# Kernel optimization log

Hardware: AMD Instinct MI355X
Metric: run time of the kernel (lower is better)

Reference implementation:

```python
import jax, jax.numpy as jnp
import numpy as np

N_NODES = 50000
N_EDGES = 1600000
L = 16  # lifted_dim

def setup_inputs() -> dict:
    key = jax.random.key(0)
    ks = jax.random.split(key, 12)
    M1 = 2 * L          # 32
    M2 = 4 * M1 + 2 * L  # 160
    s = lambda f: 1.0 / np.sqrt(f)
    return {
        "x_s": jax.random.normal(ks[0], (N_NODES, L), jnp.float32),
        "x_t": jax.random.normal(ks[1], (N_NODES, L), jnp.float32),
        "edge_attr": jax.random.normal(ks[2], (N_EDGES, L), jnp.float32),
        "u": jax.random.normal(ks[3], (1, L), jnp.float32),
        "W1a": jax.random.normal(ks[4], (M1, M1), jnp.float32) * s(M1),
        "b1a": jnp.zeros((M1,), jnp.float32),
        "W2a": jax.random.normal(ks[5], (M1, M1), jnp.float32) * s(M1),
        "b2a": jnp.zeros((M1,), jnp.float32),
        "W1b": jax.random.normal(ks[6], (M2, M2), jnp.float32) * s(M2),
        "b1b": jnp.zeros((M2,), jnp.float32),
        "W2b": jax.random.normal(ks[7], (M2, L), jnp.float32) * s(M2),
        "b2b": jnp.zeros((L,), jnp.float32),
        "gamma": jnp.ones((L,), jnp.float32),
        "beta": jnp.zeros((L,), jnp.float32),
        "edge_index": jax.random.randint(ks[8], (2, N_EDGES), 0, N_NODES, jnp.int32),
    }

def _leaky(x, slope):
    return jnp.where(x >= 0, x, slope * x)

def _forward(x_s, x_t, edge_attr, u, W1a, b1a, W2a, b2a, W1b, b1b, W2b, b2b, gamma, beta, edge_index):
    src, tgt = edge_index[0], edge_index[1]
    n = x_s.shape[0]
    # message MLP on gathered neighbor features
    in_msg = jnp.concatenate([x_t[tgt], edge_attr], axis=1)          # [E, 2L]
    h = _leaky(in_msg @ W1a + b1a, 0.1)
    msg = h @ W2a + b2a                                              # [E, 2L]
    # multi-moment segment reduce
    seg = lambda v: jax.ops.segment_sum(v, src, num_segments=n)
    cnt = seg(jnp.ones((msg.shape[0], 1), msg.dtype))
    denom = jnp.maximum(cnt, 1.0)
    mean = seg(msg) / denom                                          # [N, 2L]
    var = _leaky(seg(msg * msg) / denom - mean * mean, 0.01)
    std = jnp.sqrt(var + 1e-6)
    z = (msg - mean[src]) / std[src]                                 # standardized per-edge
    skew = jnp.nan_to_num(seg(z ** 3) / denom, nan=0.0)
    kurt = jnp.nan_to_num(seg(z ** 4) / denom, nan=0.0)
    h_cat = jnp.concatenate([x_s, mean, std, skew, kurt,
                             jnp.broadcast_to(u, (n, u.shape[1]))], axis=-1)  # [N, 10L]
    h2 = _leaky(h_cat @ W1b + b1b, 0.1)
    out = h2 @ W2b + b2b                                             # [N, L]
    # BatchNorm1d (training-mode batch stats, eps=1e-5)
    mu = jnp.mean(out, axis=0)
    vb = jnp.mean((out - mu) ** 2, axis=0)
    return gamma * (out - mu) * jax.lax.rsqrt(vb + 1e-5) + beta

def reference(x_s, x_t, edge_attr, u, W1a, b1a, W2a, b2a, W1b, b1b, W2b, b2b, gamma, beta, edge_index):
    return _forward(x_s, x_t, edge_attr, u, W1a, b1a, W2a, b2a, W1b, b1b, W2b, b2b, gamma, beta, edge_index)
```

## Files before the change

### kernel.cpp

```cpp
#include <hip/hip_runtime.h>

#define N_NODES 50000
#define N_EDGES 1600000

#define EPB 8192
#define NB1 ((N_EDGES + EPB - 1) / EPB)
#define NPB 64
#define NBK ((N_NODES + NPB - 1) / NPB)
#define TBL (NBK * NB1)
#define NSB ((TBL + 255) / 256)
#define MAXB 4096
#define SCATB 1024

typedef unsigned short ushort_t;
typedef __attribute__((ext_vector_type(8))) __bf16 bf16x8;
typedef __attribute__((ext_vector_type(4))) float  f32x4;

union FU { ushort_t s[8]; bf16x8 v; };

__device__ __forceinline__ ushort_t f2bf(float f) {
    union { float f; unsigned int i; } v; v.f = f;
    unsigned int r = v.i + 0x7fffu + ((v.i >> 16) & 1u);
    return (ushort_t)(r >> 16);
}
__device__ __forceinline__ float leaky(float x, float s) { return x >= 0.f ? x : s * x; }

__global__ __launch_bounds__(256) void k_cvtx(const float* __restrict__ x_t,
                                              ushort_t* __restrict__ x_tb) {
    int i = blockIdx.x * 256 + threadIdx.x;
    if (i < (N_NODES * 16) / 4) {
        f32x4 v = ((const f32x4*)x_t)[i];
        unsigned long long p = (unsigned long long)f2bf(v[0])
                             | ((unsigned long long)f2bf(v[1]) << 16)
                             | ((unsigned long long)f2bf(v[2]) << 32)
                             | ((unsigned long long)f2bf(v[3]) << 48);
        ((unsigned long long*)x_tb)[i] = p;
    }
}

__global__ __launch_bounds__(SCATB) void k_bcount(const int* __restrict__ src, int* __restrict__ table) {
    __shared__ int cnt[NBK];
    const int t = threadIdx.x, blk = blockIdx.x;
    for (int i = t; i < NBK; i += SCATB) cnt[i] = 0;
    __syncthreads();
    const int base = blk * EPB;
    for (int i = t; i < EPB; i += SCATB) {
        int e = base + i;
        if (e < N_EDGES) atomicAdd(&cnt[src[e] >> 6], 1);
    }
    __syncthreads();
    for (int b = t; b < NBK; b += SCATB) table[b * NB1 + blk] = cnt[b];
}

__global__ __launch_bounds__(256) void k_scan1(int* __restrict__ table, int* __restrict__ bsum) {
    __shared__ int buf[256];
    const int t = threadIdx.x, i = blockIdx.x * 256 + t;
    int v = (i < TBL) ? table[i] : 0;
    buf[t] = v; __syncthreads();
    for (int off = 1; off < 256; off <<= 1) {
        int x = (t >= off) ? buf[t - off] : 0;
        __syncthreads(); buf[t] += x; __syncthreads();
    }
    int incl = buf[t];
    if (i < TBL) table[i] = incl - v;
    if (t == 255) bsum[blockIdx.x] = incl;
}
__global__ __launch_bounds__(256) void k_scan2(int* __restrict__ bsum, float* __restrict__ bnsum) {
    __shared__ int sums[256];
    const int t = threadIdx.x;
    if (t < 32) bnsum[t] = 0.f;
    const int SEG = (NSB + 255) / 256;
    const int s0 = t * SEG, s1 = (s0 + SEG < NSB) ? s0 + SEG : NSB;
    int sum = 0;
    for (int i = s0; i < s1; i++) sum += bsum[i];
    sums[t] = sum; __syncthreads();
    for (int off = 1; off < 256; off <<= 1) {
        int x = (t >= off) ? sums[t - off] : 0;
        __syncthreads(); sums[t] += x; __syncthreads();
    }
    int carry = sums[t] - sum;
    for (int i = s0; i < s1; i++) { int v = bsum[i]; bsum[i] = carry; carry += v; }
}
__global__ __launch_bounds__(256) void k_scan3(int* __restrict__ table, const int* __restrict__ bsum) {
    const int i = blockIdx.x * 256 + threadIdx.x;
    if (i < TBL) table[i] += bsum[blockIdx.x];
}

__global__ __launch_bounds__(SCATB) void k_bscat(const int* __restrict__ src, const int* __restrict__ tgt,
                                                 const float* __restrict__ ea, const int* __restrict__ table,
                                                 int* __restrict__ tnA, ushort_t* __restrict__ eaA) {
    __shared__ int cur[NBK];
    const int t = threadIdx.x, blk = blockIdx.x;
    for (int i = t; i < NBK; i += SCATB) cur[i] = table[i * NB1 + blk];
    __syncthreads();
    const int base = blk * EPB;
    for (int i = t; i < EPB; i += SCATB) {
        int e = base + i;
        if (e < N_EDGES) {
            int s = src[e];
            int pos = atomicAdd(&cur[s >> 6], 1);
            tnA[pos] = tgt[e] | ((s & (NPB - 1)) << 16);
            const f32x4* ep = (const f32x4*)(ea + (size_t)e * 16);
            f32x4 v0 = __builtin_nontemporal_load(ep);
            f32x4 v1 = __builtin_nontemporal_load(ep + 1);
            f32x4 v2 = __builtin_nontemporal_load(ep + 2);
            f32x4 v3 = __builtin_nontemporal_load(ep + 3);
            FU lo, hi;
            #pragma unroll
            for (int j = 0; j < 4; j++) {
                lo.s[j] = f2bf(v0[j]); lo.s[4 + j] = f2bf(v1[j]);
                hi.s[j] = f2bf(v2[j]); hi.s[4 + j] = f2bf(v3[j]);
            }
            *(bf16x8*)(eaA + (size_t)pos * 16)     = lo.v;
            *(bf16x8*)(eaA + (size_t)pos * 16 + 8) = hi.v;
        }
    }
}

__global__ __launch_bounds__(256) void k_nodeF(
    const ushort_t* __restrict__ x_tb, const ushort_t* __restrict__ eaA, const int* __restrict__ tnA,
    const int* __restrict__ table,
    const float* __restrict__ w1a, const float* __restrict__ b1a,
    const float* __restrict__ w2a, const float* __restrict__ b2a,
    const float* __restrict__ x_s, const float* __restrict__ u,
    ushort_t* __restrict__ hcat)
{
    __shared__ ushort_t permL[MAXB];
    __shared__ ushort_t tgL[MAXB];
    __shared__ int cntL[NPB], scanL[NPB], curL[NPB];
    __shared__ __align__(16) float h_lds[4][16][36];
    __shared__ ushort_t stat_lds[4][128];

    const int t = threadIdx.x;
    const int w = t >> 6, L = t & 63, q = L >> 4, c = L & 15;
    const int b = blockIdx.x;
    const int base  = table[b * NB1];
    const int end   = (b < NBK - 1) ? table[(b + 1) * NB1] : N_EDGES;
    const int cntB0 = end - base;
    const int cntB  = cntB0 < MAXB ? cntB0 : MAXB;

    if (t < NPB) cntL[t] = 0;
    __syncthreads();
    for (int i = t; i < cntB; i += 256) {
        int v = tnA[base + i];
        tgL[i] = (ushort_t)(v & 0xFFFF);
        atomicAdd(&cntL[v >> 16], 1);
    }
    __syncthreads();
    if (t == 0) {
        int s = 0;
        for (int nl = 0; nl < NPB; nl++) { scanL[nl] = s; s += cntL[nl]; }
    }
    __syncthreads();
    if (t < NPB) curL[t] = scanL[t];
    __syncthreads();
    for (int i = t; i < cntB; i += 256) {
        int nl = tnA[base + i] >> 16;
        int loc = atomicAdd(&curL[nl], 1);
        permL[loc] = (ushort_t)i;
    }

    bf16x8 B1[2], B2[2];
    #pragma unroll
    for (int h = 0; h < 2; h++) {
        FU u1, u2;
        #pragma unroll
        for (int j = 0; j < 8; j++) {
            int kk = q * 8 + j, nn = c + 16 * h;
            u1.s[j] = f2bf(w1a[kk * 32 + nn]);
            u2.s[j] = f2bf(w2a[kk * 32 + nn]);
        }
        B1[h] = u1.v; B2[h] = u2.v;
    }
    const float bias1[2] = { b1a[c], b1a[c + 16] };
    const float bias2[2] = { b2a[c], b2a[c + 16] };
    const f32x4 zero = { 0.f, 0.f, 0.f, 0.f };
    __syncthreads();

    for (int kn = 0; kn < 16; kn++) {
        const int nl = w * 16 + kn;
        const int n  = b * NPB + nl;
        const int startL = scanL[nl], d = cntL[nl];
        float s1a = 0.f, s2a = 0.f, s3a = 0.f, s4a = 0.f;
        float s1b = 0.f, s2b = 0.f, s3b = 0.f, s4b = 0.f;
        const int ntl = (d + 15) >> 4;

        for (int tl = 0; tl < ntl; tl++) {
            int row  = tl * 16 + c;
            int ridx = row < d ? row : d - 1;
            int li   = permL[startL + ridx];
            FU af;
            if (q < 2) {
                int tg = tgL[li];
                __builtin_memcpy(&af.v, x_tb + (size_t)tg * 16 + q * 8, 16);
            } else {
                __builtin_memcpy(&af.v, eaA + (size_t)(base + li) * 16 + (q - 2) * 8, 16);
            }

            f32x4 a0 = __builtin_amdgcn_mfma_f32_16x16x32_bf16(af.v, B1[0], zero, 0, 0, 0);
            f32x4 a1 = __builtin_amdgcn_mfma_f32_16x16x32_bf16(af.v, B1[1], zero, 0, 0, 0);
            #pragma unroll
            for (int r = 0; r < 4; r++) {
                h_lds[w][q * 4 + r][c]      = leaky(a0[r] + bias1[0], 0.1f);
                h_lds[w][q * 4 + r][c + 16] = leaky(a1[r] + bias1[1], 0.1f);
            }
            __asm__ volatile("s_waitcnt lgkmcnt(0)" ::: "memory");

            float hv[8];
            __builtin_memcpy(&hv, &h_lds[w][c][q * 8], 32);
            FU hf;
            #pragma unroll
            for (int j = 0; j < 8; j++) hf.s[j] = f2bf(hv[j]);
            f32x4 m0 = __builtin_amdgcn_mfma_f32_16x16x32_bf16(hf.v, B2[0], zero, 0, 0, 0);
            f32x4 m1 = __builtin_amdgcn_mfma_f32_16x16x32_bf16(hf.v, B2[1], zero, 0, 0, 0);

            int rb = tl * 16 + q * 4;
            #pragma unroll
            for (int r = 0; r < 4; r++) {
                if (rb + r < d) {
                    float m = m0[r] + bias2[0], mm = m * m;
                    s1a += m;  s2a += mm; s3a += mm * m; s4a += mm * mm;
                    float x = m1[r] + bias2[1], xx = x * x;
                    s1b += x;  s2b += xx; s3b += xx * x; s4b += xx * xx;
                }
            }
        }

        if (n >= N_NODES) continue;

        s1a += __shfl_xor(s1a, 16); s1a += __shfl_xor(s1a, 32);
        s2a += __shfl_xor(s2a, 16); s2a += __shfl_xor(s2a, 32);
        s3a += __shfl_xor(s3a, 16); s3a += __shfl_xor(s3a, 32);
        s4a += __shfl_xor(s4a, 16); s4a += __shfl_xor(s4a, 32);
        s1b += __shfl_xor(s1b, 16); s1b += __shfl_xor(s1b, 32);
        s2b += __shfl_xor(s2b, 16); s2b += __shfl_xor(s2b, 32);
        s3b += __shfl_xor(s3b, 16); s3b += __shfl_xor(s3b, 32);
        s4b += __shfl_xor(s4b, 16); s4b += __shfl_xor(s4b, 32);

        if (q == 0) {
            float denom = fmaxf((float)d, 1.f);
            {
                float mean = s1a / denom, m2r = s2a / denom, m3r = s3a / denom, m4r = s4a / denom;
                float var  = leaky(m2r - mean * mean, 0.01f);
                float stdv = sqrtf(var + 1e-6f);
                float e3   = m3r - 3.f * mean * m2r + 2.f * mean * mean * mean;
                float skew = e3 / (stdv * stdv * stdv);
                float e4   = m4r - 4.f * mean * m3r + 6.f * mean * mean * m2r
                             - 3.f * mean * mean * mean * mean;
                float kurt = e4 / (stdv * stdv * stdv * stdv);
                stat_lds[w][c]      = f2bf(mean);
                stat_lds[w][32 + c] = f2bf(stdv);
                stat_lds[w][64 + c] = f2bf(skew);
                stat_lds[w][96 + c] = f2bf(kurt);
            }
            {
                float mean = s1b / denom, m2r = s2b / denom, m3r = s3b / denom, m4r = s4b / denom;
                float var  = leaky(m2r - mean * mean, 0.01f);
                float stdv = sqrtf(var + 1e-6f);
                float e3   = m3r - 3.f * mean * m2r + 2.f * mean * mean * mean;
                float skew = e3 / (stdv * stdv * stdv);
                float e4   = m4r - 4.f * mean * m3r + 6.f * mean * mean * m2r
                             - 3.f * mean * mean * mean * mean;
                float kurt = e4 / (stdv * stdv * stdv * stdv);
                stat_lds[w][16 + c]  = f2bf(mean);
                stat_lds[w][48 + c]  = f2bf(stdv);
                stat_lds[w][80 + c]  = f2bf(skew);
                stat_lds[w][112 + c] = f2bf(kurt);
            }
        }
        __asm__ volatile("s_waitcnt lgkmcnt(0)" ::: "memory");

        const size_t basep = (size_t)n * 160;
        unsigned int sv;
        __builtin_memcpy(&sv, &stat_lds[w][L * 2], 4);
        *(unsigned int*)(hcat + basep + 16 + L * 2) = sv;
        if (L < 16) {
            hcat[basep + L]       = f2bf(x_s[(size_t)n * 16 + L]);
            hcat[basep + 144 + L] = f2bf(u[L]);
        }
    }
}

__global__ __launch_bounds__(256) void k_gemm1(const ushort_t* __restrict__ hcat,
                                               const float* __restrict__ w1b,
                                               const float* __restrict__ b1b,
                                               ushort_t* __restrict__ h2)
{
    __shared__ __align__(16) ushort_t W1T[160 * 168];
    int t = threadIdx.x;
    for (int i = t; i < 160 * 160; i += 256) { int k = i / 160, n = i % 160; W1T[n * 168 + k] = f2bf(w1b[i]); }
    __syncthreads();
    int w = t >> 6, L = t & 63, q = L >> 4, c = L & 15;
    const f32x4 zero = { 0.f, 0.f, 0.f, 0.f };
    for (int tile = blockIdx.x * 4 + w; tile < 3125 * 10; tile += gridDim.x * 4) {
        int rt = tile / 10, nt = tile % 10;
        int m = rt * 16 + c, n = nt * 16 + c;
        f32x4 acc = zero;
        #pragma unroll
        for (int ks = 0; ks < 5; ks++) {
            bf16x8 a; __builtin_memcpy(&a, hcat + (size_t)m * 160 + ks * 32 + q * 8, 16);
            bf16x8 b; __builtin_memcpy(&b, &W1T[n * 168 + ks * 32 + q * 8], 16);
            acc = __builtin_amdgcn_mfma_f32_16x16x32_bf16(a, b, acc, 0, 0, 0);
        }
        float bias = b1b[n];
        #pragma unroll
        for (int r = 0; r < 4; r++) {
            h2[(size_t)(rt * 16 + q * 4 + r) * 160 + n] = f2bf(leaky(acc[r] + bias, 0.1f));
        }
    }
}

__global__ __launch_bounds__(256) void k_gemm2(const ushort_t* __restrict__ h2,
                                               const float* __restrict__ w2b,
                                               const float* __restrict__ b2b,
                                               float* __restrict__ outpre, float* __restrict__ bnsum)
{
    __shared__ __align__(16) ushort_t W2T[16 * 168];
    int t = threadIdx.x;
    for (int i = t; i < 160 * 16; i += 256) { int k = i / 16, n = i % 16; W2T[n * 168 + k] = f2bf(w2b[i]); }
    __syncthreads();
    int w = t >> 6, L = t & 63, q = L >> 4, c = L & 15;
    const f32x4 zero = { 0.f, 0.f, 0.f, 0.f };
    float ps = 0.f, ps2 = 0.f;
    float bias = b2b[c];
    for (int rt = blockIdx.x * 4 + w; rt < 3125; rt += gridDim.x * 4) {
        int m = rt * 16 + c;
        f32x4 acc = zero;
        #pragma unroll
        for (int ks = 0; ks < 5; ks++) {
            bf16x8 a; __builtin_memcpy(&a, h2 + (size_t)m * 160 + ks * 32 + q * 8, 16);
            bf16x8 b; __builtin_memcpy(&b, &W2T[c * 168 + ks * 32 + q * 8], 16);
            acc = __builtin_amdgcn_mfma_f32_16x16x32_bf16(a, b, acc, 0, 0, 0);
        }
        #pragma unroll
        for (int r = 0; r < 4; r++) {
            float v = acc[r] + bias;
            outpre[(size_t)(rt * 16 + q * 4 + r) * 16 + c] = v;
            ps += v; ps2 += v * v;
        }
    }
    ps  += __shfl_xor(ps, 16);  ps  += __shfl_xor(ps, 32);
    ps2 += __shfl_xor(ps2, 16); ps2 += __shfl_xor(ps2, 32);
    if (q == 0) {
        unsafeAtomicAdd(&bnsum[c], ps);
        unsafeAtomicAdd(&bnsum[16 + c], ps2);
    }
}

__global__ __launch_bounds__(256) void k_bn(const float* __restrict__ outpre, const float* __restrict__ bnsum,
                                            const float* __restrict__ gamma, const float* __restrict__ beta,
                                            float* __restrict__ out)
{
    int i = blockIdx.x * 256 + threadIdx.x;
    int c = i & 15;
    float x = outpre[i];
    float mu = bnsum[c] * (1.f / N_NODES);
    float var = bnsum[16 + c] * (1.f / N_NODES) - mu * mu;
    out[i] = gamma[c] * (x - mu) * rsqrtf(var + 1e-5f) + beta[c];
}

extern "C" void kernel_launch(void* const* d_in, const int* in_sizes, int n_in,
                              void* d_out, int out_size, void* d_ws, size_t ws_size,
                              hipStream_t stream) {
    const float* x_s  = (const float*)d_in[0];
    const float* x_t  = (const float*)d_in[1];
    const float* ea   = (const float*)d_in[2];
    const float* u    = (const float*)d_in[3];
    const float* w1a  = (const float*)d_in[4];
    const float* b1a  = (const float*)d_in[5];
    const float* w2a  = (const float*)d_in[6];
    const float* b2a  = (const float*)d_in[7];
    const float* w1b  = (const float*)d_in[8];
    const float* b1b  = (const float*)d_in[9];
    const float* w2b  = (const float*)d_in[10];
    const float* b2b  = (const float*)d_in[11];
    const float* gam  = (const float*)d_in[12];
    const float* bet  = (const float*)d_in[13];
    const int* eidx   = (const int*)d_in[14];
    const int* src = eidx;
    const int* tgt = eidx + N_EDGES;

    char* ws = (char*)d_ws;
    const size_t OFF_TABLE  = 0;
    const size_t OFF_BSUM   = 614400;
    const size_t OFF_BNSUM  = 655360;
    const size_t OFF_OUTPRE = 786432;
    const size_t OFF_XTB    = 4194304;
    const size_t OFF_TNA    = 6291456;
    const size_t OFF_EAA    = 16777216;
    const size_t OFF_HCAT   = 68157440;
    const size_t OFF_H2     = 84934656;

    int*      table  = (int*)(ws + OFF_TABLE);
    int*      bsum   = (int*)(ws + OFF_BSUM);
    float*    bnsum  = (float*)(ws + OFF_BNSUM);
    float*    outpre = (float*)(ws + OFF_OUTPRE);
    ushort_t* x_tb   = (ushort_t*)(ws + OFF_XTB);
    int*      tnA    = (int*)(ws + OFF_TNA);
    ushort_t* eaA    = (ushort_t*)(ws + OFF_EAA);
    ushort_t* hcat   = (ushort_t*)(ws + OFF_HCAT);
    ushort_t* h2     = (ushort_t*)(ws + OFF_H2);

    k_cvtx  <<<(N_NODES * 16 / 4 + 255) / 256, 256, 0, stream>>>(x_t, x_tb);
    k_bcount<<<NB1, SCATB, 0, stream>>>(src, table);
    k_scan1 <<<NSB, 256, 0, stream>>>(table, bsum);
    k_scan2 <<<1,   256, 0, stream>>>(bsum, bnsum);
    k_scan3 <<<NSB, 256, 0, stream>>>(table, bsum);
    k_bscat <<<NB1, SCATB, 0, stream>>>(src, tgt, ea, table, tnA, eaA);
    k_nodeF <<<NBK, 256, 0, stream>>>(x_tb, eaA, tnA, table, w1a, b1a, w2a, b2a, x_s, u, hcat);
    k_gemm1 <<<1024, 256, 0, stream>>>(hcat, w1b, b1b, h2);
    k_gemm2 <<<512,  256, 0, stream>>>(h2, w2b, b2b, outpre, bnsum);
    k_bn    <<<(N_NODES * 16) / 256, 256, 0, stream>>>(outpre, bnsum, gam, bet, (float*)d_out);
}
```

Measured before the change: 429.9 us.

## Fuse x_t conversion and scan fix-up into consumers, double nodes per block

The x_t-to-bf16 conversion moves into the bucket-count kernel, and the separate scan3 pass is removed: consumers now add the block prefix from bsum when they read the table. Node buckets grow from 64 to 128 nodes, and the node kernel runs 512 threads with LDS scratch sized for 8 waves. This cuts two launches and halves the number of node blocks and table entries. The cost is more LDS and threads per block, and a per-bucket edge cap that could overflow on skewed inputs.

```diff
diff --git a/kernel.cpp b/kernel.cpp
--- a/kernel.cpp
+++ b/kernel.cpp
@@ -5,12 +5,13 @@
 
 #define EPB 8192
 #define NB1 ((N_EDGES + EPB - 1) / EPB)
-#define NPB 64
+#define NPB 128
 #define NBK ((N_NODES + NPB - 1) / NPB)
 #define TBL (NBK * NB1)
 #define NSB ((TBL + 255) / 256)
-#define MAXB 4096
+#define MAXB 4608
 #define SCATB 1024
+#define NFT 512
 
 typedef unsigned short ushort_t;
 typedef __attribute__((ext_vector_type(8))) __bf16 bf16x8;
@@ -25,28 +26,25 @@
 }
 __device__ __forceinline__ float leaky(float x, float s) { return x >= 0.f ? x : s * x; }
 
-__global__ __launch_bounds__(256) void k_cvtx(const float* __restrict__ x_t,
-                                              ushort_t* __restrict__ x_tb) {
-    int i = blockIdx.x * 256 + threadIdx.x;
-    if (i < (N_NODES * 16) / 4) {
-        f32x4 v = ((const f32x4*)x_t)[i];
+__global__ __launch_bounds__(SCATB) void k_bcount(const int* __restrict__ src, int* __restrict__ table,
+                                                  const float* __restrict__ x_t, ushort_t* __restrict__ x_tb) {
+    __shared__ int cnt[NBK];
+    const int t = threadIdx.x, blk = blockIdx.x;
+    const int g = blk * SCATB + t;
+    if (g < (N_NODES * 16) / 4) {
+        f32x4 v = ((const f32x4*)x_t)[g];
         unsigned long long p = (unsigned long long)f2bf(v[0])
                              | ((unsigned long long)f2bf(v[1]) << 16)
                              | ((unsigned long long)f2bf(v[2]) << 32)
                              | ((unsigned long long)f2bf(v[3]) << 48);
-        ((unsigned long long*)x_tb)[i] = p;
-    }
-}
-
-__global__ __launch_bounds__(SCATB) void k_bcount(const int* __restrict__ src, int* __restrict__ table) {
-    __shared__ int cnt[NBK];
-    const int t = threadIdx.x, blk = blockIdx.x;
+        ((unsigned long long*)x_tb)[g] = p;
+    }
     for (int i = t; i < NBK; i += SCATB) cnt[i] = 0;
     __syncthreads();
     const int base = blk * EPB;
     for (int i = t; i < EPB; i += SCATB) {
         int e = base + i;
-        if (e < N_EDGES) atomicAdd(&cnt[src[e] >> 6], 1);
+        if (e < N_EDGES) atomicAdd(&cnt[src[e] >> 7], 1);
     }
     __syncthreads();
     for (int b = t; b < NBK; b += SCATB) table[b * NB1 + blk] = cnt[b];
@@ -81,24 +79,24 @@
     int carry = sums[t] - sum;
     for (int i = s0; i < s1; i++) { int v = bsum[i]; bsum[i] = carry; carry += v; }
 }
-__global__ __launch_bounds__(256) void k_scan3(int* __restrict__ table, const int* __restrict__ bsum) {
-    const int i = blockIdx.x * 256 + threadIdx.x;
-    if (i < TBL) table[i] += bsum[blockIdx.x];
-}
 
 __global__ __launch_bounds__(SCATB) void k_bscat(const int* __restrict__ src, const int* __restrict__ tgt,
                                                  const float* __restrict__ ea, const int* __restrict__ table,
+                                                 const int* __restrict__ bsum,
                                                  int* __restrict__ tnA, ushort_t* __restrict__ eaA) {
     __shared__ int cur[NBK];
     const int t = threadIdx.x, blk = blockIdx.x;
-    for (int i = t; i < NBK; i += SCATB) cur[i] = table[i * NB1 + blk];
+    for (int i = t; i < NBK; i += SCATB) {
+        int idx = i * NB1 + blk;
+        cur[i] = table[idx] + bsum[idx >> 8];
+    }
     __syncthreads();
     const int base = blk * EPB;
     for (int i = t; i < EPB; i += SCATB) {
         int e = base + i;
         if (e < N_EDGES) {
             int s = src[e];
-            int pos = atomicAdd(&cur[s >> 6], 1);
+            int pos = atomicAdd(&cur[s >> 7], 1);
             tnA[pos] = tgt[e] | ((s & (NPB - 1)) << 16);
             const f32x4* ep = (const f32x4*)(ea + (size_t)e * 16);
             f32x4 v0 = __builtin_nontemporal_load(ep);
@@ -117,9 +115,9 @@
     }
 }
 
-__global__ __launch_bounds__(256) void k_nodeF(
+__global__ __launch_bounds__(NFT) void k_nodeF(
     const ushort_t* __restrict__ x_tb, const ushort_t* __restrict__ eaA, const int* __restrict__ tnA,
-    const int* __restrict__ table,
+    const int* __restrict__ table, const int* __restrict__ bsum,
     const float* __restrict__ w1a, const float* __restrict__ b1a,
     const float* __restrict__ w2a, const float* __restrict__ b2a,
     const float* __restrict__ x_s, const float* __restrict__ u,
@@ -128,20 +126,23 @@
     __shared__ ushort_t permL[MAXB];
     __shared__ ushort_t tgL[MAXB];
     __shared__ int cntL[NPB], scanL[NPB], curL[NPB];
-    __shared__ __align__(16) float h_lds[4][16][36];
-    __shared__ ushort_t stat_lds[4][128];
+    __shared__ __align__(16) float h_lds[8][16][36];
+    __shared__ ushort_t stat_lds[8][128];
 
     const int t = threadIdx.x;
     const int w = t >> 6, L = t & 63, q = L >> 4, c = L & 15;
     const int b = blockIdx.x;
-    const int base  = table[b * NB1];
-    const int end   = (b < NBK - 1) ? table[(b + 1) * NB1] : N_EDGES;
+    const int i0   = b * NB1;
+    const int base = table[i0] + bsum[i0 >> 8];
+    int end;
+    if (b < NBK - 1) { const int i1 = (b + 1) * NB1; end = table[i1] + bsum[i1 >> 8]; }
+    else end = N_EDGES;
     const int cntB0 = end - base;
     const int cntB  = cntB0 < MAXB ? cntB0 : MAXB;
 
     if (t < NPB) cntL[t] = 0;
     __syncthreads();
-    for (int i = t; i < cntB; i += 256) {
+    for (int i = t; i < cntB; i += NFT) {
         int v = tnA[base + i];
         tgL[i] = (ushort_t)(v & 0xFFFF);
         atomicAdd(&cntL[v >> 16], 1);
@@ -154,7 +155,7 @@
     __syncthreads();
     if (t < NPB) curL[t] = scanL[t];
     __syncthreads();
-    for (int i = t; i < cntB; i += 256) {
+    for (int i = t; i < cntB; i += NFT) {
         int nl = tnA[base + i] >> 16;
         int loc = atomicAdd(&curL[nl], 1);
         permL[loc] = (ushort_t)i;
@@ -401,13 +402,11 @@
     ushort_t* hcat   = (ushort_t*)(ws + OFF_HCAT);
     ushort_t* h2     = (ushort_t*)(ws + OFF_H2);
 
-    k_cvtx  <<<(N_NODES * 16 / 4 + 255) / 256, 256, 0, stream>>>(x_t, x_tb);
-    k_bcount<<<NB1, SCATB, 0, stream>>>(src, table);
+    k_bcount<<<NB1, SCATB, 0, stream>>>(src, table, x_t, x_tb);
     k_scan1 <<<NSB, 256, 0, stream>>>(table, bsum);
     k_scan2 <<<1,   256, 0, stream>>>(bsum, bnsum);
-    k_scan3 <<<NSB, 256, 0, stream>>>(table, bsum);
-    k_bscat <<<NB1, SCATB, 0, stream>>>(src, tgt, ea, table, tnA, eaA);
-    k_nodeF <<<NBK, 256, 0, stream>>>(x_tb, eaA, tnA, table, w1a, b1a, w2a, b2a, x_s, u, hcat);
+    k_bscat <<<NB1, SCATB, 0, stream>>>(src, tgt, ea, table, bsum, tnA, eaA);
+    k_nodeF <<<NBK, NFT, 0, stream>>>(x_tb, eaA, tnA, table, bsum, w1a, b1a, w2a, b2a, x_s, u, hcat);
     k_gemm1 <<<1024, 256, 0, stream>>>(hcat, w1b, b1b, h2);
     k_gemm2 <<<512,  256, 0, stream>>>(h2, w2b, b2b, outpre, bnsum);
     k_bn    <<<(N_NODES * 16) / 256, 256, 0, stream>>>(outpre, bnsum, gam, bet, (float*)d_out);
```

After: 415.5 us. 3.3% less time.
